# Kernel optimization log

Hardware: AMD Instinct MI355X
Metric: run time of the kernel (lower is better)

Reference implementation:

```python
import jax, jax.numpy as jnp
import numpy as np

B, N, C, H = 4, 4096, 1024, 16
HD = C // H  # head_dim = 64
EPS = 1e-6


def setup_inputs() -> dict:
    key = jax.random.key(0)
    ks = jax.random.split(key, 5)
    x = jax.random.normal(ks[0], (B, N, C), dtype=jnp.float32)
    s_in = 1.0 / np.sqrt(C)
    W_qkv = jax.random.normal(ks[1], (C, 3 * C), dtype=jnp.float32) * s_in
    b_qkv = jnp.zeros((3 * C,), dtype=jnp.float32)
    W_out = jax.random.normal(ks[2], (C, C), dtype=jnp.float32) * s_in
    b_out = jnp.zeros((C,), dtype=jnp.float32)
    return {"x": x, "W_qkv": W_qkv, "b_qkv": b_qkv, "W_out": W_out, "b_out": b_out}


def reference(x, W_qkv, b_qkv, W_out, b_out):
    # qkv projection: (B, N, 3C)
    qkv = jnp.einsum('bnc,cf->bnf', x, W_qkv) + b_qkv
    # rearrange 'b n (h d) -> b h n d' with d = 3*head_dim, then chunk into q,k,v
    qkv = qkv.reshape(B, N, H, 3 * HD).transpose(0, 2, 1, 3)  # (B,H,N,3*HD)
    q, k, v = jnp.split(qkv, 3, axis=-1)  # each (B,H,N,HD)
    # silu feature map
    q = jax.nn.silu(q)
    k = jax.nn.silu(k)
    # linear attention: state = k^T @ v per head  -> (B,H,HD,HD)
    state = jnp.einsum('bhnd,bhne->bhde', k, v)
    k_sum = k.sum(axis=2)  # (B,H,HD)
    num = jnp.einsum('bhnd,bhde->bhne', q, state)  # (B,H,N,HD)
    den = jnp.einsum('bhnd,bhd->bhn', q, k_sum)[..., None]  # (B,H,N,1)
    out = num / (den + EPS)
    # 'b h n d -> b n (h d)'
    out = out.transpose(0, 2, 1, 3).reshape(B, N, C)
    return jnp.einsum('bnc,cf->bnf', out, W_out) + b_out
```

## Files before the change

kernel.cpp:

```cpp
#include <hip/hip_runtime.h>

typedef unsigned short u16;
typedef unsigned int u32;
typedef __attribute__((ext_vector_type(8))) short short8;
typedef __attribute__((ext_vector_type(8))) _Float16 half8;
typedef __attribute__((ext_vector_type(4))) float f32x4;

#define DEV __device__ __forceinline__

DEV void async_copy16(const void* g, void* l) {
  __builtin_amdgcn_global_load_lds((const __attribute__((address_space(1))) u32*)g,
                                   (__attribute__((address_space(3))) u32*)l, 16, 0, 0);
}
DEV float bf2f(u16 u) { return __uint_as_float(((u32)u) << 16); }
DEV u16 f2bf(float f) {
  u32 x = __float_as_uint(f);
  return (u16)((x + 0x7fffu + ((x >> 16) & 1u)) >> 16);
}
DEV u16 f2h_bits(float f) { _Float16 h = (_Float16)f; return __builtin_bit_cast(u16, h); }
DEV float h2f_bits(u16 b) { return (float)__builtin_bit_cast(_Float16, b); }
DEV float silu_f(float x) { return x / (1.0f + __expf(-x)); }

DEV void stage_tile(const u16* __restrict__ G, size_t grow_base, int k0, u16* L, int t) {
#pragma unroll
  for (int it = 0; it < 2; ++it) {
    int c = t + it * 256;
    int r = c >> 2, j = c & 3;
    int js = j ^ ((r >> 1) & 3);
    async_copy16(G + ((grow_base + (size_t)r) << 10) + k0 + js * 8,
                 (char*)L + (size_t)c * 16);
  }
}
DEV half8 frag(const u16* L, int rr, int lq) {
  int sw = lq ^ ((rr >> 1) & 3);
  return *(const half8*)((const char*)L + (size_t)rr * 64 + sw * 16);
}
DEV short8 frag_s(const u16* L, int rr, int lq) {
  int sw = lq ^ ((rr >> 1) & 3);
  return *(const short8*)((const char*)L + (size_t)rr * 64 + sw * 16);
}
DEV half8 frag64(const u16* L, int rr, int slot) {
  return *(const half8*)(L + (size_t)rr * 64 + ((slot ^ (rr & 7)) * 8));
}

__global__ __launch_bounds__(256) void transpose_k(const float* __restrict__ W,
                                                   u16* __restrict__ Wt,
                                                   int K, int N) {
  __shared__ float s[32][33];
  int t = threadIdx.x;
  int tx = t & 31, ty = t >> 5;
  int ntk = K >> 5;
  int bk = blockIdx.x % ntk, bn = blockIdx.x / ntk;
  int k0 = bk * 32, n0 = bn * 32;
#pragma unroll
  for (int i = 0; i < 4; ++i)
    s[ty + 8 * i][tx] = W[(size_t)(k0 + ty + 8 * i) * N + n0 + tx];
  __syncthreads();
#pragma unroll
  for (int i = 0; i < 4; ++i) {
    int r = ty + 8 * i;
    Wt[(size_t)(n0 + r) * K + k0 + tx] = f2bf(s[tx][r]);
  }
}

__global__ __launch_bounds__(256) void prep(const float* __restrict__ x,
                                            u16* __restrict__ X0, u16* __restrict__ X1,
                                            const float* __restrict__ Wq,
                                            u16* __restrict__ W0t, u16* __restrict__ W1t,
                                            const float* __restrict__ Wo,
                                            u16* __restrict__ WoT) {
  __shared__ float s[32][33];
  int bid = blockIdx.x, t = threadIdx.x;
  if (bid < 16384) {
    int i = (bid * 256 + t) * 4;
    float4 v = *(const float4*)&x[i];
    ushort4 h0, h1;
    h0.x = f2h_bits(v.x); h1.x = f2h_bits((v.x - h2f_bits(h0.x)) * 4096.0f);
    h0.y = f2h_bits(v.y); h1.y = f2h_bits((v.y - h2f_bits(h0.y)) * 4096.0f);
    h0.z = f2h_bits(v.z); h1.z = f2h_bits((v.z - h2f_bits(h0.z)) * 4096.0f);
    h0.w = f2h_bits(v.w); h1.w = f2h_bits((v.w - h2f_bits(h0.w)) * 4096.0f);
    *(ushort4*)&X0[i] = h0;
    *(ushort4*)&X1[i] = h1;
  } else if (bid < 16384 + 3072) {
    int b2 = bid - 16384;
    int tx = t & 31, ty = t >> 5;
    int bk = b2 & 31, bn = b2 >> 5;
    int k0 = bk * 32, n0 = bn * 32;
#pragma unroll
    for (int i = 0; i < 4; ++i)
      s[ty + 8 * i][tx] = Wq[(size_t)(k0 + ty + 8 * i) * 3072 + n0 + tx];
    __syncthreads();
#pragma unroll
    for (int i = 0; i < 4; ++i) {
      int r = ty + 8 * i;
      int col = n0 + r;
      int h = col / 192, rem = col - h * 192;
      int cty = rem >> 6, d = rem & 63;
      int pcol = cty * 1024 + h * 64 + d;
      float v = s[tx][r];
      u16 h0 = f2h_bits(v);
      u16 h1 = f2h_bits((v - h2f_bits(h0)) * 4096.0f);
      size_t o = (size_t)pcol * 1024 + k0 + tx;
      W0t[o] = h0;
      W1t[o] = h1;
    }
  } else {
    int b3 = bid - 19456;
    int tx = t & 31, ty = t >> 5;
    int bk = b3 & 31, bn = b3 >> 5;
    int k0 = bk * 32, n0 = bn * 32;
#pragma unroll
    for (int i = 0; i < 4; ++i)
      s[ty + 8 * i][tx] = Wo[(size_t)(k0 + ty + 8 * i) * 1024 + n0 + tx];
    __syncthreads();
#pragma unroll
    for (int i = 0; i < 4; ++i) {
      int r = ty + 8 * i;
      WoT[(size_t)(n0 + r) * 1024 + k0 + tx] = f2bf(s[tx][r]);
    }
  }
}

__global__ __launch_bounds__(256, 2) void gemm_qk_f16(
    const u16* __restrict__ X0, const u16* __restrict__ X1,
    const u16* __restrict__ W0, const u16* __restrict__ W1,
    const float* __restrict__ bq,
    float* __restrict__ Qf, u16* __restrict__ Kt, float* __restrict__ ksumP2) {
  __shared__ u16 lA0[2][128 * 32];
  __shared__ u16 lA1[2][128 * 32];
  __shared__ u16 lB0[2][128 * 32];
  __shared__ u16 lB1[2][128 * 32];
  int t = threadIdx.x;
  int w = t >> 6, l = t & 63;
  int wr = w >> 1, wc = w & 1;
  int lr = l & 15, lq = l >> 4;
  int mb = blockIdx.y * 128, nb = blockIdx.x * 128;
  int cty = nb >> 10;
  f32x4 aM[4][4] = {};
  f32x4 aC[4][4] = {};

  for (int k0 = 0; k0 < 1024; k0 += 64) {
#pragma unroll
    for (int kk = 0; kk < 2; ++kk) {
#pragma unroll
      for (int it = 0; it < 2; ++it) {
        int c = t + it * 256;
        int r = c >> 2, j = c & 3;
        int js = j ^ ((r >> 1) & 3);
        size_t goA = (((size_t)(mb + r)) << 10) + k0 + kk * 32 + js * 8;
        size_t goB = (((size_t)(nb + r)) << 10) + k0 + kk * 32 + js * 8;
        async_copy16(X0 + goA, (char*)lA0[kk] + (size_t)c * 16);
        async_copy16(X1 + goA, (char*)lA1[kk] + (size_t)c * 16);
        async_copy16(W0 + goB, (char*)lB0[kk] + (size_t)c * 16);
        async_copy16(W1 + goB, (char*)lB1[kk] + (size_t)c * 16);
      }
    }
    __syncthreads();
#pragma unroll
    for (int kk = 0; kk < 2; ++kk) {
      half8 b0[4], b1[4];
#pragma unroll
      for (int nn = 0; nn < 4; ++nn) {
        int rr = wc * 64 + nn * 16 + lr;
        b0[nn] = frag(lB0[kk], rr, lq);
        b1[nn] = frag(lB1[kk], rr, lq);
      }
#pragma unroll
      for (int m = 0; m < 4; ++m) {
        int rr = wr * 64 + m * 16 + lr;
        half8 a0 = frag(lA0[kk], rr, lq);
        half8 a1 = frag(lA1[kk], rr, lq);
#pragma unroll
        for (int nn = 0; nn < 4; ++nn) {
          aM[m][nn] = __builtin_amdgcn_mfma_f32_16x16x32_f16(a0, b0[nn], aM[m][nn], 0, 0, 0);
          aC[m][nn] = __builtin_amdgcn_mfma_f32_16x16x32_f16(a0, b1[nn], aC[m][nn], 0, 0, 0);
          aC[m][nn] = __builtin_amdgcn_mfma_f32_16x16x32_f16(a1, b0[nn], aC[m][nn], 0, 0, 0);
        }
      }
    }
    __syncthreads();
  }

  const float cscale = 2.44140625e-4f;
  if (cty == 0) {
#pragma unroll
    for (int nn = 0; nn < 4; ++nn) {
      int col = nb + wc * 64 + nn * 16 + lr;
      int h = (col & 1023) >> 6, d0 = col & 63;
      float bias = bq[h * 192 + d0];
#pragma unroll
      for (int m = 0; m < 4; ++m)
#pragma unroll
        for (int j = 0; j < 4; ++j) {
          int row = mb + wr * 64 + m * 16 + lq * 4 + j;
          int b = row >> 12, n = row & 4095;
          size_t base = (((size_t)(b * 16 + h) * 4096 + n) << 6) + d0;
          float val = aM[m][nn][j] + aC[m][nn][j] * cscale + bias;
          Qf[base] = silu_f(val);
        }
    }
  } else {
    float* red = (float*)lA0;
    int b = mb >> 12, nbase = mb & 4095;
#pragma unroll
    for (int nn = 0; nn < 4; ++nn) {
      int clocal = wc * 64 + nn * 16 + lr;
      int colk = (nb - 1024) + clocal;
      int h = colk >> 6, d0 = colk & 63;
      float bias = bq[h * 192 + 64 + d0];
      size_t krow = (((size_t)(b * 16 + h) * 64 + d0) << 12) + nbase + wr * 64;
      float lsum = 0.0f;
#pragma unroll
      for (int m = 0; m < 4; ++m) {
        ushort4 pk;
        float v0 = silu_f(aM[m][nn][0] + aC[m][nn][0] * cscale + bias);
        float v1 = silu_f(aM[m][nn][1] + aC[m][nn][1] * cscale + bias);
        float v2 = silu_f(aM[m][nn][2] + aC[m][nn][2] * cscale + bias);
        float v3 = silu_f(aM[m][nn][3] + aC[m][nn][3] * cscale + bias);
        lsum += v0 + v1 + v2 + v3;
        pk.x = f2bf(v0); pk.y = f2bf(v1); pk.z = f2bf(v2); pk.w = f2bf(v3);
        *(ushort4*)&Kt[krow + m * 16 + lq * 4] = pk;
      }
      red[clocal * 8 + wr * 4 + lq] = lsum;
    }
    __syncthreads();
    if (t < 128) {
      float s = 0.0f;
#pragma unroll
      for (int c = 0; c < 8; ++c) s += red[t * 8 + c];
      int colk = (nb - 1024) + t;
      int h = colk >> 6, d0 = colk & 63;
      int rowtile = blockIdx.y & 31;
      ksumP2[(((size_t)(b * 16 + h) * 64 + d0) << 5) + rowtile] = s;
    }
  }
}

__global__ __launch_bounds__(256) void gemm_v_f16(
    const u16* __restrict__ X0, const u16* __restrict__ W0,
    const float* __restrict__ bq, u16* __restrict__ Vt) {
  __shared__ u16 lA0[2][128 * 32];
  __shared__ u16 lB0[2][128 * 32];
  int t = threadIdx.x;
  int w = t >> 6, l = t & 63;
  int wr = w >> 1, wc = w & 1;
  int lr = l & 15, lq = l >> 4;
  int mb = blockIdx.y * 128, nb = 2048 + blockIdx.x * 128;
  f32x4 aM[4][4] = {};

  for (int k0 = 0; k0 < 1024; k0 += 64) {
    stage_tile(X0, mb, k0, lA0[0], t);
    stage_tile(X0, mb, k0 + 32, lA0[1], t);
    stage_tile(W0, nb, k0, lB0[0], t);
    stage_tile(W0, nb, k0 + 32, lB0[1], t);
    __syncthreads();
#pragma unroll
    for (int kk = 0; kk < 2; ++kk) {
      half8 b0[4];
#pragma unroll
      for (int nn = 0; nn < 4; ++nn) b0[nn] = frag(lB0[kk], wc * 64 + nn * 16 + lr, lq);
#pragma unroll
      for (int m = 0; m < 4; ++m) {
        half8 a0 = frag(lA0[kk], wr * 64 + m * 16 + lr, lq);
#pragma unroll
        for (int nn = 0; nn < 4; ++nn)
          aM[m][nn] = __builtin_amdgcn_mfma_f32_16x16x32_f16(a0, b0[nn], aM[m][nn], 0, 0, 0);
      }
    }
    __syncthreads();
  }
  int b = mb >> 12, nbase = mb & 4095;
#pragma unroll
  for (int nn = 0; nn < 4; ++nn) {
    int colv = (nb - 2048) + wc * 64 + nn * 16 + lr;
    int h = colv >> 6, e0 = colv & 63;
    float bias = bq[h * 192 + 128 + e0];
    size_t vrow = (((size_t)(b * 16 + h) * 64 + e0) << 12) + nbase + wr * 64;
#pragma unroll
    for (int m = 0; m < 4; ++m) {
      ushort4 pk;
      pk.x = f2bf(aM[m][nn][0] + bias);
      pk.y = f2bf(aM[m][nn][1] + bias);
      pk.z = f2bf(aM[m][nn][2] + bias);
      pk.w = f2bf(aM[m][nn][3] + bias);
      *(ushort4*)&Vt[vrow + m * 16 + lq * 4] = pk;
    }
  }
}

__global__ __launch_bounds__(256) void state_mfma(const u16* __restrict__ Kt,
                                                  const u16* __restrict__ Vt,
                                                  float* __restrict__ stateP) {
  __shared__ u16 sA[64 * 32];
  __shared__ u16 sB[64 * 32];
  int bh = blockIdx.y, ch = blockIdx.x, t = threadIdx.x;
  int w = t >> 6, l = t & 63;
  int wr = w >> 1, wc = w & 1;
  int lr = l & 15, lq = l >> 4;
  size_t rb = (size_t)bh << 6;
  f32x4 acc[2][2] = {};

  for (int n0 = ch * 512; n0 < ch * 512 + 512; n0 += 32) {
    {
      int c = t;
      int r = c >> 2, j = c & 3;
      int js = j ^ ((r >> 1) & 3);
      size_t go = ((rb + (size_t)r) << 12) + n0 + js * 8;
      async_copy16(Kt + go, (char*)sA + (size_t)c * 16);
      async_copy16(Vt + go, (char*)sB + (size_t)c * 16);
    }
    __syncthreads();
    short8 bfr[2];
#pragma unroll
    for (int nn = 0; nn < 2; ++nn) bfr[nn] = frag_s(sB, wc * 32 + nn * 16 + lr, lq);
#pragma unroll
    for (int m = 0; m < 2; ++m) {
      short8 a = frag_s(sA, wr * 32 + m * 16 + lr, lq);
#pragma unroll
      for (int nn = 0; nn < 2; ++nn)
        acc[m][nn] = __builtin_amdgcn_mfma_f32_16x16x32_bf16(a, bfr[nn], acc[m][nn], 0, 0, 0);
    }
    __syncthreads();
  }

  size_t pb = ((size_t)bh * 8 + ch) * 4096;
#pragma unroll
  for (int m = 0; m < 2; ++m)
#pragma unroll
    for (int nn = 0; nn < 2; ++nn)
#pragma unroll
      for (int j = 0; j < 4; ++j) {
        int d = wr * 32 + m * 16 + lq * 4 + j;
        int e = wc * 32 + nn * 16 + lr;
        stateP[pb + (size_t)d * 64 + e] = acc[m][nn][j];
      }
}

__global__ __launch_bounds__(256) void reduce_state2(const float* __restrict__ stateP,
                                                     const float* __restrict__ ksumP2,
                                                     u16* __restrict__ sTh,
                                                     float* __restrict__ ksumF) {
  int bh = blockIdx.x, t = threadIdx.x;
#pragma unroll
  for (int i = 0; i < 16; ++i) {
    int idx = t + i * 256;
    float s = 0.0f;
#pragma unroll
    for (int c = 0; c < 8; ++c) s += stateP[((size_t)bh * 8 + c) * 4096 + idx];
    int d = idx >> 6, e = idx & 63;
    sTh[((size_t)bh << 12) + e * 64 + d] = f2h_bits(s);
  }
  if (t < 64) {
    float s = 0.0f;
#pragma unroll
    for (int c = 0; c < 32; ++c) s += ksumP2[(((size_t)bh * 64 + t) << 5) + c];
    ksumF[(size_t)bh * 64 + t] = s;
  }
}

__global__ __launch_bounds__(256) void attn_mfma(const float* __restrict__ Qf,
                                                 const u16* __restrict__ sTh,
                                                 const float* __restrict__ ksumF,
                                                 u16* __restrict__ outb) {
  __shared__ u16 q16[256 * 64];
  __shared__ u16 sT[64 * 64];
  __shared__ float denp[256 * 4];
  __shared__ float den[256];
  int bh = blockIdx.y, chnk = blockIdx.x, t = threadIdx.x;
  int w = t >> 6, l = t & 63;
  int lr16 = l & 15, lq4 = l >> 4;

  {
    const u16* src = sTh + ((size_t)bh << 12);
#pragma unroll
    for (int it = 0; it < 2; ++it) {
      int c = t + it * 256;
      short8 v = *(const short8*)(src + c * 8);
      int e = c >> 3, slot = c & 7;
      *(short8*)&sT[e * 64 + ((slot ^ (e & 7)) * 8)] = v;
    }
  }
  {
    int quarter = t & 3, rbase = t >> 2;
    float4 skr[4];
#pragma unroll
    for (int i4 = 0; i4 < 4; ++i4)
      skr[i4] = *(const float4*)&ksumF[(size_t)bh * 64 + quarter * 16 + i4 * 4];
#pragma unroll
    for (int p = 0; p < 4; ++p) {
      int row = rbase + p * 64;
      int n = chnk * 256 + row;
      const float* qrow = Qf + (((size_t)bh * 4096 + n) << 6) + quarter * 16;
      float dp = 0.0f;
      u16 h[16];
#pragma unroll
      for (int i4 = 0; i4 < 4; ++i4) {
        float4 v = *(const float4*)(qrow + i4 * 4);
        dp += v.x * skr[i4].x + v.y * skr[i4].y + v.z * skr[i4].z + v.w * skr[i4].w;
        h[i4 * 4 + 0] = f2h_bits(v.x);
        h[i4 * 4 + 1] = f2h_bits(v.y);
        h[i4 * 4 + 2] = f2h_bits(v.z);
        h[i4 * 4 + 3] = f2h_bits(v.w);
      }
      denp[row * 4 + quarter] = dp;
      int s0 = (quarter * 2) ^ (row & 7);
      int s1 = (quarter * 2 + 1) ^ (row & 7);
      *(short8*)&q16[row * 64 + s0 * 8] = *(short8*)&h[0];
      *(short8*)&q16[row * 64 + s1 * 8] = *(short8*)&h[8];
    }
  }
  __syncthreads();
  den[t] = denp[t * 4] + denp[t * 4 + 1] + denp[t * 4 + 2] + denp[t * 4 + 3];
  __syncthreads();

  f32x4 acc[4][4] = {};
#pragma unroll
  for (int kh = 0; kh < 2; ++kh) {
    half8 bfr[4];
#pragma unroll
    for (int nt = 0; nt < 4; ++nt)
      bfr[nt] = frag64(sT, nt * 16 + lr16, kh * 4 + lq4);
#pragma unroll
    for (int rt = 0; rt < 4; ++rt) {
      half8 a = frag64(q16, w * 64 + rt * 16 + lr16, kh * 4 + lq4);
#pragma unroll
      for (int nt = 0; nt < 4; ++nt)
        acc[rt][nt] = __builtin_amdgcn_mfma_f32_16x16x32_f16(a, bfr[nt], acc[rt][nt], 0, 0, 0);
    }
  }

  int b = bh >> 4, hh = bh & 15;
#pragma unroll
  for (int rt = 0; rt < 4; ++rt) {
#pragma unroll
    for (int j = 0; j < 4; ++j) {
      int row = w * 64 + rt * 16 + lq4 * 4 + j;
      float rden = 1.0f / (den[row] + 1e-6f);
      int n = chnk * 256 + row;
      size_t ob = (((size_t)(b * 4096 + n)) << 10) + hh * 64;
#pragma unroll
      for (int nt = 0; nt < 4; ++nt) {
        int e = nt * 16 + lr16;
        outb[ob + e] = f2bf(acc[rt][nt][j] * rden);
      }
    }
  }
}

__global__ __launch_bounds__(256) void gemm_out(const u16* __restrict__ A,
                                                const u16* __restrict__ Bt,
                                                const float* __restrict__ bias,
                                                float* __restrict__ C) {
  __shared__ u16 lA[2][128 * 32];
  __shared__ u16 lB[2][128 * 32];
  int t = threadIdx.x;
  int w = t >> 6, l = t & 63;
  int wr = w >> 1, wc = w & 1;
  int lr = l & 15, lq = l >> 4;
  int mb = blockIdx.y * 128, nb = blockIdx.x * 128;
  f32x4 acc[4][4] = {};

  for (int k0 = 0; k0 < 1024; k0 += 64) {
    stage_tile(A, mb, k0, lA[0], t);
    stage_tile(A, mb, k0 + 32, lA[1], t);
    stage_tile(Bt, nb, k0, lB[0], t);
    stage_tile(Bt, nb, k0 + 32, lB[1], t);
    __syncthreads();
#pragma unroll
    for (int kk = 0; kk < 2; ++kk) {
      short8 af[4], bf[4];
#pragma unroll
      for (int m = 0; m < 4; ++m) af[m] = frag_s(lA[kk], wr * 64 + m * 16 + lr, lq);
#pragma unroll
      for (int nn = 0; nn < 4; ++nn) bf[nn] = frag_s(lB[kk], wc * 64 + nn * 16 + lr, lq);
#pragma unroll
      for (int m = 0; m < 4; ++m)
#pragma unroll
        for (int nn = 0; nn < 4; ++nn)
          acc[m][nn] = __builtin_amdgcn_mfma_f32_16x16x32_bf16(af[m], bf[nn], acc[m][nn], 0, 0, 0);
    }
    __syncthreads();
  }

#pragma unroll
  for (int m = 0; m < 4; ++m)
#pragma unroll
    for (int nn = 0; nn < 4; ++nn) {
      int col = nb + wc * 64 + nn * 16 + lr;
      float bc = bias[col];
#pragma unroll
      for (int j = 0; j < 4; ++j) {
        int row = mb + wr * 64 + m * 16 + lq * 4 + j;
        C[((size_t)row << 10) + col] = acc[m][nn][j] + bc;
      }
    }
}

__global__ __launch_bounds__(256) void gemm_qkv(const float* __restrict__ X,
                                                const float* __restrict__ Wq,
                                                const float* __restrict__ bq,
                                                float* __restrict__ Qf,
                                                float* __restrict__ Kf,
                                                u16* __restrict__ Vb) {
  __shared__ float sA[16 * 132];
  __shared__ float sB[16 * 128];
  int t = threadIdx.x;
  int tm = t >> 4, tn = t & 15;
  int mb = blockIdx.y * 128, nb = blockIdx.x * 128;
  float acc[8][8] = {};

  for (int k0 = 0; k0 < 1024; k0 += 16) {
#pragma unroll
    for (int it = 0; it < 2; ++it) {
      int c = t + it * 256;
      int m = c >> 2, kc = (c & 3) * 4;
      float4 v = *(const float4*)&X[(size_t)(mb + m) * 1024 + k0 + kc];
      sA[(kc + 0) * 132 + m] = v.x;
      sA[(kc + 1) * 132 + m] = v.y;
      sA[(kc + 2) * 132 + m] = v.z;
      sA[(kc + 3) * 132 + m] = v.w;
      int kr = c >> 5, nc = (c & 31) * 4;
      async_copy16(&Wq[(size_t)(k0 + kr) * 3072 + nb + nc], (char*)sB + (size_t)c * 16);
    }
    __syncthreads();
#pragma unroll
    for (int k = 0; k < 16; ++k) {
      float4 a0 = *(const float4*)&sA[k * 132 + tm * 8];
      float4 a1 = *(const float4*)&sA[k * 132 + tm * 8 + 4];
      float4 b0 = *(const float4*)&sB[k * 128 + tn * 8];
      float4 b1 = *(const float4*)&sB[k * 128 + tn * 8 + 4];
      const float av[8] = {a0.x, a0.y, a0.z, a0.w, a1.x, a1.y, a1.z, a1.w};
      const float bv[8] = {b0.x, b0.y, b0.z, b0.w, b1.x, b1.y, b1.z, b1.w};
#pragma unroll
      for (int i = 0; i < 8; ++i)
#pragma unroll
        for (int j = 0; j < 8; ++j) acc[i][j] = fmaf(av[i], bv[j], acc[i][j]);
    }
    __syncthreads();
  }

  int c0 = nb + tn * 8;
  int h = c0 / 192, rem = c0 % 192;
  int ty = rem >> 6, d0 = rem & 63;
  float bb[8];
#pragma unroll
  for (int j = 0; j < 8; ++j) bb[j] = bq[c0 + j];
#pragma unroll
  for (int i = 0; i < 8; ++i) {
    int r = mb + tm * 8 + i;
    int b = r >> 12, n = r & 4095;
    size_t base = (((size_t)(b * 16 + h) * 4096 + n) << 6) + d0;
    if (ty == 2) {
      u16 pk[8];
#pragma unroll
      for (int j = 0; j < 8; ++j) pk[j] = f2bf(acc[i][j] + bb[j]);
      *(short8*)&Vb[base] = *(short8*)pk;
    } else {
      float* dst = (ty == 0) ? Qf : Kf;
#pragma unroll
      for (int j = 0; j < 8; ++j) dst[base + j] = silu_f(acc[i][j] + bb[j]);
    }
  }
}

__global__ __launch_bounds__(256) void state_partial(const float* __restrict__ Kf,
                                                     const u16* __restrict__ Vb,
                                                     float* __restrict__ stateP,
                                                     float* __restrict__ ksumP) {
  int bh = blockIdx.y, ch = blockIdx.x, t = threadIdx.x;
  __shared__ float sK[64 * 64];
  __shared__ u16 sV[64 * 64];
  __shared__ float sred[256];
  int n0 = ch * 512;
  size_t base = ((size_t)bh * 4096 + n0) << 6;
  float acc[4][4] = {};
  int te = t & 15, td = t >> 4;
  int kd = t & 63, kq = t >> 6;
  float kacc = 0.0f;

  for (int sc = 0; sc < 8; ++sc) {
    const float* gk = Kf + base + (size_t)sc * 64 * 64;
    const u16* gv = Vb + base + (size_t)sc * 64 * 64;
#pragma unroll
    for (int it = 0; it < 4; ++it)
      async_copy16(gk + (size_t)(t + it * 256) * 4, (char*)sK + (size_t)(t + it * 256) * 16);
#pragma unroll
    for (int it = 0; it < 2; ++it)
      async_copy16(gv + (size_t)(t + it * 256) * 8, (char*)sV + (size_t)(t + it * 256) * 16);
    __syncthreads();
#pragma unroll 4
    for (int n = 0; n < 64; ++n) {
      float4 k4 = *(const float4*)&sK[n * 64 + td * 4];
      const float ka[4] = {k4.x, k4.y, k4.z, k4.w};
      ushort4 vv = *(const ushort4*)&sV[n * 64 + te * 4];
      const float va[4] = {bf2f(vv.x), bf2f(vv.y), bf2f(vv.z), bf2f(vv.w)};
#pragma unroll
      for (int i = 0; i < 4; ++i)
#pragma unroll
        for (int j = 0; j < 4; ++j) acc[i][j] = fmaf(ka[i], va[j], acc[i][j]);
    }
#pragma unroll
    for (int i = 0; i < 16; ++i) kacc += sK[(kq * 16 + i) * 64 + kd];
    __syncthreads();
  }
  size_t pb = ((size_t)bh * 8 + ch) * 4096;
#pragma unroll
  for (int i = 0; i < 4; ++i)
#pragma unroll
    for (int j = 0; j < 4; ++j)
      stateP[pb + (size_t)(td * 4 + i) * 64 + te * 4 + j] = acc[i][j];

  sred[t] = kacc;
  __syncthreads();
  if (t < 64)
    ksumP[((size_t)bh * 8 + ch) * 64 + t] = sred[t] + sred[t + 64] + sred[t + 128] + sred[t + 192];
}

__global__ __launch_bounds__(256) void reduce_state_fb(const float* __restrict__ stateP,
                                                       const float* __restrict__ ksumP,
                                                       u16* __restrict__ sTh,
                                                       float* __restrict__ ksumF) {
  int bh = blockIdx.x, t = threadIdx.x;
#pragma unroll
  for (int i = 0; i < 16; ++i) {
    int idx = t + i * 256;
    float s = 0.0f;
#pragma unroll
    for (int c = 0; c < 8; ++c) s += stateP[((size_t)bh * 8 + c) * 4096 + idx];
    int d = idx >> 6, e = idx & 63;
    sTh[((size_t)bh << 12) + e * 64 + d] = f2h_bits(s);
  }
  if (t < 64) {
    float s = 0.0f;
#pragma unroll
    for (int c = 0; c < 8; ++c) s += ksumP[((size_t)bh * 8 + c) * 64 + t];
    ksumF[(size_t)bh * 64 + t] = s;
  }
}

extern "C" void kernel_launch(void* const* d_in, const int* in_sizes, int n_in,
                              void* d_out, int out_size, void* d_ws, size_t ws_size,
                              hipStream_t stream) {
  const float* x    = (const float*)d_in[0];
  const float* Wqkv = (const float*)d_in[1];
  const float* bqkv = (const float*)d_in[2];
  const float* Wout = (const float*)d_in[3];
  const float* bout = (const float*)d_in[4];
  float* out = (float*)d_out;

  char* w = (char*)d_ws;

  const size_t fKT  = 0;
  const size_t fVT  = fKT  + 33554432ULL;
  const size_t fSP  = fVT  + 33554432ULL;
  const size_t fKP2 = fSP  + 8388608ULL;
  const size_t fWT  = fKP2 + 524288ULL;
  const size_t fST  = fWT  + 2097152ULL;
  const size_t fKF  = fST  + 524288ULL;
  const size_t fX0  = fKF  + 16384ULL;
  const size_t fX1  = fX0  + 33554432ULL;
  const size_t fW0  = fX1  + 33554432ULL;
  const size_t fW1  = fW0  + 6291456ULL;
  const size_t need_fast = fW1 + 6291456ULL;

  const size_t bK  = 0;
  const size_t bV  = bK + 67108864ULL;
  const size_t bSP = bV + 33554432ULL;
  const size_t bKP = bSP + 8388608ULL;
  const size_t bWT = bKP + 131072ULL;
  const size_t bST = bWT + 2097152ULL;
  const size_t bKF = bST + 524288ULL;
  const size_t need_base = bKF + 16384ULL;

  if (ws_size >= need_fast) {
    u16*   Kt     = (u16*)(w + fKT);
    u16*   outb   = (u16*)(w + fKT);
    u16*   Vt     = (u16*)(w + fVT);
    float* stateP = (float*)(w + fSP);
    float* ksumP2 = (float*)(w + fKP2);
    u16*   WoutT  = (u16*)(w + fWT);
    u16*   sTh    = (u16*)(w + fST);
    float* ksumF  = (float*)(w + fKF);
    u16*   X0     = (u16*)(w + fX0);
    u16*   X1     = (u16*)(w + fX1);
    u16*   W0     = (u16*)(w + fW0);
    u16*   W1     = (u16*)(w + fW1);
    float* Qf     = out;

    prep<<<dim3(20480), dim3(256), 0, stream>>>(x, X0, X1, Wqkv, W0, W1, Wout, WoutT);
    gemm_qk_f16<<<dim3(16, 128), dim3(256), 0, stream>>>(X0, X1, W0, W1, bqkv, Qf, Kt, ksumP2);
    gemm_v_f16<<<dim3(8, 128), dim3(256), 0, stream>>>(X0, W0, bqkv, Vt);
    state_mfma<<<dim3(8, 64), dim3(256), 0, stream>>>(Kt, Vt, stateP);
    reduce_state2<<<dim3(64), dim3(256), 0, stream>>>(stateP, ksumP2, sTh, ksumF);
    attn_mfma<<<dim3(16, 64), dim3(256), 0, stream>>>(Qf, sTh, ksumF, outb);
    gemm_out<<<dim3(8, 128), dim3(256), 0, stream>>>(outb, WoutT, bout, out);
  } else if (ws_size >= need_base) {
    float* Kf     = (float*)(w + bK);
    u16*   outb   = (u16*)(w + bK);
    u16*   Vb     = (u16*)(w + bV);
    float* stateP = (float*)(w + bSP);
    float* ksumP  = (float*)(w + bKP);
    u16*   WoutT  = (u16*)(w + bWT);
    u16*   sTh    = (u16*)(w + bST);
    float* ksumF  = (float*)(w + bKF);
    float* Qf     = out;

    transpose_k<<<dim3(1024), dim3(256), 0, stream>>>(Wout, WoutT, 1024, 1024);
    gemm_qkv<<<dim3(24, 128), dim3(256), 0, stream>>>(x, Wqkv, bqkv, Qf, Kf, Vb);
    state_partial<<<dim3(8, 64), dim3(256), 0, stream>>>(Kf, Vb, stateP, ksumP);
    reduce_state_fb<<<dim3(64), dim3(256), 0, stream>>>(stateP, ksumP, sTh, ksumF);
    attn_mfma<<<dim3(16, 64), dim3(256), 0, stream>>>(Qf, sTh, ksumF, outb);
    gemm_out<<<dim3(8, 128), dim3(256), 0, stream>>>(outb, WoutT, bout, out);
  }
}
```

Before: 395.4 us.

## Double-buffer QK GEMM K-loop to overlap async LDS loads with MFMA

```diff
diff --git a/kernel.cpp b/kernel.cpp
--- a/kernel.cpp
+++ b/kernel.cpp
@@ -139,47 +139,58 @@
   f32x4 aM[4][4] = {};
   f32x4 aC[4][4] = {};
 
-  for (int k0 = 0; k0 < 1024; k0 += 64) {
-#pragma unroll
-    for (int kk = 0; kk < 2; ++kk) {
-#pragma unroll
-      for (int it = 0; it < 2; ++it) {
-        int c = t + it * 256;
-        int r = c >> 2, j = c & 3;
-        int js = j ^ ((r >> 1) & 3);
-        size_t goA = (((size_t)(mb + r)) << 10) + k0 + kk * 32 + js * 8;
-        size_t goB = (((size_t)(nb + r)) << 10) + k0 + kk * 32 + js * 8;
-        async_copy16(X0 + goA, (char*)lA0[kk] + (size_t)c * 16);
-        async_copy16(X1 + goA, (char*)lA1[kk] + (size_t)c * 16);
-        async_copy16(W0 + goB, (char*)lB0[kk] + (size_t)c * 16);
-        async_copy16(W1 + goB, (char*)lB1[kk] + (size_t)c * 16);
+#define QK_STAGE(B, K0)                                                  \
+  {                                                                      \
+    _Pragma("unroll")                                                    \
+    for (int it_ = 0; it_ < 2; ++it_) {                                  \
+      int c_ = t + it_ * 256;                                            \
+      int r_ = c_ >> 2, j_ = c_ & 3;                                     \
+      int js_ = j_ ^ ((r_ >> 1) & 3);                                    \
+      size_t goA_ = (((size_t)(mb + r_)) << 10) + (K0) + js_ * 8;        \
+      size_t goB_ = (((size_t)(nb + r_)) << 10) + (K0) + js_ * 8;        \
+      async_copy16(X0 + goA_, (char*)lA0[B] + (size_t)c_ * 16);          \
+      async_copy16(X1 + goA_, (char*)lA1[B] + (size_t)c_ * 16);          \
+      async_copy16(W0 + goB_, (char*)lB0[B] + (size_t)c_ * 16);          \
+      async_copy16(W1 + goB_, (char*)lB1[B] + (size_t)c_ * 16);          \
+    }                                                                    \
+  }
+
+  QK_STAGE(0, 0);
+  int cur = 0;
+  for (int k0 = 0; k0 < 1024; k0 += 32) {
+    if (k0 + 32 < 1024) {
+      QK_STAGE(cur ^ 1, k0 + 32);
+      asm volatile("s_waitcnt vmcnt(8)" ::: "memory");
+    } else {
+      asm volatile("s_waitcnt vmcnt(0)" ::: "memory");
+    }
+    __builtin_amdgcn_sched_barrier(0);
+    __builtin_amdgcn_s_barrier();
+    __builtin_amdgcn_sched_barrier(0);
+    half8 b0[4], b1[4];
+#pragma unroll
+    for (int nn = 0; nn < 4; ++nn) {
+      int rr = wc * 64 + nn * 16 + lr;
+      b0[nn] = frag(lB0[cur], rr, lq);
+      b1[nn] = frag(lB1[cur], rr, lq);
+    }
+#pragma unroll
+    for (int m = 0; m < 4; ++m) {
+      int rr = wr * 64 + m * 16 + lr;
+      half8 a0 = frag(lA0[cur], rr, lq);
+      half8 a1 = frag(lA1[cur], rr, lq);
+#pragma unroll
+      for (int nn = 0; nn < 4; ++nn) {
+        aM[m][nn] = __builtin_amdgcn_mfma_f32_16x16x32_f16(a0, b0[nn], aM[m][nn], 0, 0, 0);
+        aC[m][nn] = __builtin_amdgcn_mfma_f32_16x16x32_f16(a0, b1[nn], aC[m][nn], 0, 0, 0);
+        aC[m][nn] = __builtin_amdgcn_mfma_f32_16x16x32_f16(a1, b0[nn], aC[m][nn], 0, 0, 0);
       }
     }
-    __syncthreads();
-#pragma unroll
-    for (int kk = 0; kk < 2; ++kk) {
-      half8 b0[4], b1[4];
-#pragma unroll
-      for (int nn = 0; nn < 4; ++nn) {
-        int rr = wc * 64 + nn * 16 + lr;
-        b0[nn] = frag(lB0[kk], rr, lq);
-        b1[nn] = frag(lB1[kk], rr, lq);
-      }
-#pragma unroll
-      for (int m = 0; m < 4; ++m) {
-        int rr = wr * 64 + m * 16 + lr;
-        half8 a0 = frag(lA0[kk], rr, lq);
-        half8 a1 = frag(lA1[kk], rr, lq);
-#pragma unroll
-        for (int nn = 0; nn < 4; ++nn) {
-          aM[m][nn] = __builtin_amdgcn_mfma_f32_16x16x32_f16(a0, b0[nn], aM[m][nn], 0, 0, 0);
-          aC[m][nn] = __builtin_amdgcn_mfma_f32_16x16x32_f16(a0, b1[nn], aC[m][nn], 0, 0, 0);
-          aC[m][nn] = __builtin_amdgcn_mfma_f32_16x16x32_f16(a1, b0[nn], aC[m][nn], 0, 0, 0);
-        }
-      }
-    }
-    __syncthreads();
-  }
+    __builtin_amdgcn_s_barrier();
+    __builtin_amdgcn_sched_barrier(0);
+    cur ^= 1;
+  }
+#undef QK_STAGE
 
   const float cscale = 2.44140625e-4f;
   if (cty == 0) {
```

Result: slower. 406.8 us (+2.9%).
